# Performance work log

Hardware: AMD Instinct MI355X
Metric: run time of the kernel (lower is better)

Reference implementation:

```python
import jax, jax.numpy as jnp
import numpy as np

HEADS = 8
DIM_HEAD = 64
SCALE = DIM_HEAD ** (-0.5)
EPS = 1e-5


def setup_inputs() -> dict:
    key = jax.random.key(0)
    k1, k2, k3, k4 = jax.random.split(key, 4)
    b, c, t = 16, 512, 4096
    hidden = HEADS * DIM_HEAD
    x = jax.random.normal(k1, (b, c, t), dtype=jnp.float32)
    W_qkv = jax.random.normal(k2, (hidden * 3, c), dtype=jnp.float32) * (c ** -0.5)
    W_out = jax.random.normal(k3, (c, hidden), dtype=jnp.float32) * (hidden ** -0.5)
    b_out = jax.random.normal(k4, (c,), dtype=jnp.float32) * 0.02
    gn_w = jnp.ones((c,), dtype=jnp.float32)
    gn_b = jnp.zeros((c,), dtype=jnp.float32)
    return {"x": x, "W_qkv": W_qkv, "W_out": W_out, "b_out": b_out,
            "gn_w": gn_w, "gn_b": gn_b}


def reference(x, W_qkv, W_out, b_out, gn_w, gn_b):
    b, c, t = x.shape
    # 1x1 conv = channel matmul: [3*hidden, c] @ [b, c, t] -> [b, 3*hidden, t]
    qkv = jnp.einsum('oc,bct->bot', W_qkv, x)
    q, k, v = jnp.split(qkv, 3, axis=1)
    q = q.reshape(b, HEADS, DIM_HEAD, t)
    k = k.reshape(b, HEADS, DIM_HEAD, t)
    v = v.reshape(b, HEADS, DIM_HEAD, t)
    q = jax.nn.softmax(q, axis=-2) * SCALE  # softmax over feature dim
    k = jax.nn.softmax(k, axis=-1)          # softmax over time dim
    # context = k @ v^T : [b,h,dk,t] x [b,h,t,dv] -> [b,h,dk,dv]
    context = jnp.einsum('bhdt,bhet->bhde', k, v)
    # out = context^T @ q : [b,h,dv,dk] x [b,h,dk,t] -> [b,h,dv,t]
    out = jnp.einsum('bhde,bhdt->bhet', context, q)
    out = out.reshape(b, HEADS * DIM_HEAD, t)
    # output 1x1 conv with bias
    out = jnp.einsum('oc,bct->bot', W_out, out) + b_out[None, :, None]
    # GroupNorm(1, dim): normalize over (channels, time) per sample
    mean = jnp.mean(out, axis=(1, 2), keepdims=True)
    var = jnp.var(out, axis=(1, 2), keepdims=True)
    out = (out - mean) * jax.lax.rsqrt(var + EPS)
    out = out * gn_w[None, :, None] + gn_b[None, :, None]
    return out
```

## Files before the change

### kernel.cpp

```cpp
#include <hip/hip_runtime.h>
#include <stdint.h>

#define B_ 16
#define C_ 512
#define T_ 4096
#define H_ 8
#define D_ 64
#define SCALE_ 0.125f
#define EPS_ 1e-5f

using ushortT = unsigned short;
using ushort8 = __attribute__((ext_vector_type(8))) unsigned short;
using short8  = __attribute__((ext_vector_type(8))) short;
using floatx4 = __attribute__((ext_vector_type(4))) float;

__device__ __forceinline__ float bf2f(ushortT u) {
  union { unsigned int i; float f; } x; x.i = ((unsigned int)u) << 16; return x.f;
}
__device__ __forceinline__ ushortT f2bf(float f) {
  union { float f; unsigned int i; } x; x.f = f;
  unsigned int r = x.i + 0x7fffu + ((x.i >> 16) & 1u);
  return (ushortT)(r >> 16);
}

#define GLD16(gp, lp)                                                          \
  __builtin_amdgcn_global_load_lds(                                            \
      (const __attribute__((address_space(1))) unsigned int*)(gp),             \
      (__attribute__((address_space(3))) unsigned int*)(lp), 16, 0, 0)

__global__ __launch_bounds__(256) void cvt_f32_bf16(const float* __restrict__ src,
                                                    ushortT* __restrict__ dst, int n4) {
  int i = blockIdx.x * 256 + threadIdx.x;
  if (i >= n4) return;
  floatx4 v = *(const floatx4*)(src + (size_t)i * 4);
  unsigned int p0 = (unsigned int)f2bf(v[0]) | ((unsigned int)f2bf(v[1]) << 16);
  unsigned int p1 = (unsigned int)f2bf(v[2]) | ((unsigned int)f2bf(v[3]) << 16);
  *(unsigned long long*)(dst + (size_t)i * 4) =
      (unsigned long long)p0 | ((unsigned long long)p1 << 32);
}

__global__ void zero_f32(float* p, int n4) {
  int i = blockIdx.x * 256 + threadIdx.x;
  if (i < n4) ((floatx4*)p)[i] = (floatx4){0.f, 0.f, 0.f, 0.f};
}

__global__ __launch_bounds__(256) void transpose_x(const float* __restrict__ x,
                                                   ushortT* __restrict__ xT) {
  __shared__ ushortT tile[64][65];
  int b = blockIdx.z;
  int t0 = blockIdx.x * 64, c0 = blockIdx.y * 64;
  const float* xb = x + (size_t)b * C_ * T_;
  ushortT* xTb = xT + (size_t)b * T_ * C_;
  for (int i = threadIdx.x; i < 4096; i += 256) {
    int cc = i >> 6, tt = i & 63;
    tile[cc][tt] = f2bf(xb[(size_t)(c0 + cc) * T_ + t0 + tt]);
  }
  __syncthreads();
  for (int i = threadIdx.x; i < 4096; i += 256) {
    int tt = i >> 6, cc = i & 63;
    xTb[(size_t)(t0 + tt) * C_ + c0 + cc] = tile[cc][tt];
  }
}

#define STAGE_TILE(KB, BUF)                                                    \
  {                                                                            \
    _Pragma("unroll")                                                          \
    for (int i_ = 0; i_ < 4; ++i_) {                                           \
      int wci_ = i_ * 256 + (tid & 192);                                       \
      int ci_  = wci_ + (tid & 63);                                            \
      int row_ = ci_ >> 3;                                                     \
      int scol_ = ((ci_ & 7) ^ (row_ & 7)) << 3;                               \
      GLD16(&A[(size_t)(m0 + row_) * lda + (KB) + scol_], &As[BUF][wci_ * 8]); \
      GLD16(&Bt[(size_t)(n0 + row_) * ldb + (KB) + scol_], &Bs[BUF][wci_ * 8]);\
    }                                                                          \
  }

template <int MODE>
__global__ __launch_bounds__(256) void gemm_bt(
    const ushortT* __restrict__ A, const ushortT* __restrict__ Bt,
    void* __restrict__ Cc, const float* __restrict__ bias,
    float* __restrict__ stats,
    int K, int lda, int ldb, int ldc,
    unsigned long long bsA, unsigned long long bsB, unsigned long long bsC) {
  __shared__ ushortT As[2][128 * 64];
  __shared__ ushortT Bs[2][128 * 64];
  unsigned int gx = gridDim.x, gy = gridDim.y;
  unsigned int nwg = gx * gy * gridDim.z;
  unsigned int lin = blockIdx.x + gx * (blockIdx.y + gy * blockIdx.z);
  unsigned int cpx = nwg >> 3;
  unsigned int wid = (lin & 7u) * cpx + (lin >> 3);
  unsigned int bx = wid % gx;
  unsigned int tmp = wid / gx;
  unsigned int by = tmp % gy;
  unsigned int bz = tmp / gy;

  const int b = bz;
  A += (size_t)b * bsA; Bt += (size_t)b * bsB;
  const int m0 = by * 128, n0 = bx * 128;
  const int tid = threadIdx.x;
  const int w = tid >> 6, l = tid & 63;
  const int wm = (w >> 1) * 64, wn = (w & 1) * 64;
  const int quad = l >> 4, ln = l & 15;
  floatx4 acc[4][4];
#pragma unroll
  for (int i = 0; i < 4; i++)
#pragma unroll
    for (int j = 0; j < 4; j++) acc[i][j] = (floatx4){0.f, 0.f, 0.f, 0.f};

  STAGE_TILE(0, 0);
  const int nt = K >> 6;
  for (int t = 0; t < nt; ++t) {
    const int cur = t & 1;
    if (t + 1 < nt) {
      STAGE_TILE((t + 1) << 6, cur ^ 1);
      asm volatile("s_waitcnt vmcnt(8)" ::: "memory");
    } else {
      asm volatile("s_waitcnt vmcnt(0)" ::: "memory");
    }
    __builtin_amdgcn_s_barrier();
    asm volatile("" ::: "memory");
#pragma unroll
    for (int kk = 0; kk < 2; ++kk) {
      short8 af[4], bfv[4];
#pragma unroll
      for (int i = 0; i < 4; i++)
        af[i] = *(const short8*)(
            &As[cur][(wm + i * 16 + ln) * 64 + (((kk * 4 + quad) ^ (ln & 7)) << 3)]);
#pragma unroll
      for (int j = 0; j < 4; j++)
        bfv[j] = *(const short8*)(
            &Bs[cur][(wn + j * 16 + ln) * 64 + (((kk * 4 + quad) ^ (ln & 7)) << 3)]);
#pragma unroll
      for (int i = 0; i < 4; i++)
#pragma unroll
        for (int j = 0; j < 4; j++)
          acc[i][j] = __builtin_amdgcn_mfma_f32_16x16x32_bf16(af[i], bfv[j], acc[i][j], 0, 0, 0);
    }
    asm volatile("s_waitcnt lgkmcnt(0)" ::: "memory");
    __builtin_amdgcn_s_barrier();
    asm volatile("" ::: "memory");
  }

  if constexpr (MODE == 4) {
    const bool isk = (m0 < 512);
    ushortT* Co = (ushortT*)Cc + (size_t)b * bsC;
#pragma unroll
    for (int i = 0; i < 4; i++)
#pragma unroll
      for (int r = 0; r < 4; r++) {
        int row = m0 + wm + i * 16 + quad * 4 + r;
#pragma unroll
        for (int j = 0; j < 4; j++) {
          int col = n0 + wn + j * 16 + ln;
          float v = acc[i][j][r];
          if (isk) v = expf(v);
          Co[(size_t)row * ldc + col] = f2bf(v);
        }
      }
  } else if constexpr (MODE == 2) {
    ushortT* Co = (ushortT*)Cc + (size_t)b * bsC;
#pragma unroll
    for (int i = 0; i < 4; i++)
#pragma unroll
      for (int r = 0; r < 4; r++) {
        float v0 = acc[i][0][r], v1 = acc[i][1][r], v2 = acc[i][2][r], v3 = acc[i][3][r];
        float mx = fmaxf(fmaxf(v0, v1), fmaxf(v2, v3));
#pragma unroll
        for (int off = 1; off < 16; off <<= 1) mx = fmaxf(mx, __shfl_xor(mx, off));
        float e0 = expf(v0 - mx), e1 = expf(v1 - mx);
        float e2 = expf(v2 - mx), e3 = expf(v3 - mx);
        float s = (e0 + e1) + (e2 + e3);
#pragma unroll
        for (int off = 1; off < 16; off <<= 1) s += __shfl_xor(s, off);
        float inv = SCALE_ / s;
        int row = m0 + wm + i * 16 + quad * 4 + r;
        size_t base = (size_t)row * ldc + n0 + wn + ln;
        Co[base +  0] = f2bf(e0 * inv);
        Co[base + 16] = f2bf(e1 * inv);
        Co[base + 32] = f2bf(e2 * inv);
        Co[base + 48] = f2bf(e3 * inv);
      }
  } else {
    float* Co = (float*)Cc + (size_t)b * bsC;
    float s = 0.f, ss = 0.f;
#pragma unroll
    for (int i = 0; i < 4; i++)
#pragma unroll
      for (int r = 0; r < 4; r++) {
        int row = m0 + wm + i * 16 + quad * 4 + r;
        float bv = bias ? bias[row] : 0.f;
#pragma unroll
        for (int j = 0; j < 4; j++) {
          int col = n0 + wn + j * 16 + ln;
          float v = acc[i][j][r] + bv;
          Co[(size_t)row * ldc + col] = v;
          s += v; ss += v * v;
        }
      }
#pragma unroll
    for (int off = 1; off < 64; off <<= 1) {
      s += __shfl_xor(s, off);
      ss += __shfl_xor(ss, off);
    }
    __shared__ float rs[4], rss[4];
    if (l == 0) { rs[w] = s; rss[w] = ss; }
    __syncthreads();
    if (tid == 0) {
      atomicAdd(&stats[b * 2],     rs[0] + rs[1] + rs[2] + rs[3]);
      atomicAdd(&stats[b * 2 + 1], rss[0] + rss[1] + rss[2] + rss[3]);
    }
  }
}

__global__ __launch_bounds__(64) void context_kv(const ushortT* __restrict__ kv,
                                                 float* __restrict__ ksum,
                                                 float* __restrict__ ct) {
  __shared__ ushortT Vs[64 * 32];
  __shared__ ushortT Ks[64 * 32];
  const int slice = blockIdx.x, h = blockIdx.y, b = blockIdx.z;
  const int t0 = slice * 256;
  const ushortT* vrow = kv + ((size_t)b * 1024 + 512 + h * 64) * T_;
  const ushortT* krow = kv + ((size_t)b * 1024 + h * 64) * T_;
  const int tid = threadIdx.x, quad = tid >> 4, ln = tid & 15;
  float rsum[4] = {0.f, 0.f, 0.f, 0.f};
  floatx4 acc[4][4];
#pragma unroll
  for (int i = 0; i < 4; i++)
#pragma unroll
    for (int j = 0; j < 4; j++) acc[i][j] = (floatx4){0.f, 0.f, 0.f, 0.f};
  for (int kb = 0; kb < 256; kb += 32) {
#pragma unroll
    for (int i = 0; i < 4; ++i) {
      int ci = i * 64 + tid;
      int row = ci >> 2, col = (ci & 3) << 3;
      GLD16(&vrow[(size_t)row * T_ + t0 + kb + col], &Vs[i * 512]);
      GLD16(&krow[(size_t)row * T_ + t0 + kb + col], &Ks[i * 512]);
    }
    __syncthreads();
    short8 af[4], bfv[4];
#pragma unroll
    for (int i = 0; i < 4; i++) af[i] = *(const short8*)(&Vs[(i * 16 + ln) * 32 + quad * 8]);
#pragma unroll
    for (int j = 0; j < 4; j++) {
      bfv[j] = *(const short8*)(&Ks[(j * 16 + ln) * 32 + quad * 8]);
#pragma unroll
      for (int e = 0; e < 8; e++) rsum[j] += bf2f((ushortT)bfv[j][e]);
    }
#pragma unroll
    for (int i = 0; i < 4; i++)
#pragma unroll
      for (int j = 0; j < 4; j++)
        acc[i][j] = __builtin_amdgcn_mfma_f32_16x16x32_bf16(af[i], bfv[j], acc[i][j], 0, 0, 0);
    __syncthreads();
  }
  float* ks = ksum + (size_t)b * 512 + h * 64;
#pragma unroll
  for (int j = 0; j < 4; ++j) {
    float s = rsum[j];
    s += __shfl_xor(s, 16);
    s += __shfl_xor(s, 32);
    if (quad == 0) atomicAdd(&ks[j * 16 + ln], s);
  }
  float* ctbh = ct + (size_t)(b * 8 + h) * 4096;
#pragma unroll
  for (int i = 0; i < 4; i++)
#pragma unroll
    for (int r = 0; r < 4; r++) {
      int e = i * 16 + quad * 4 + r;
#pragma unroll
      for (int j = 0; j < 4; j++) {
        int d = j * 16 + ln;
        atomicAdd(&ctbh[e * 64 + d], acc[i][j][r]);
      }
    }
}

__global__ __launch_bounds__(64) void ct_combine(const ushortT* __restrict__ Wobf,
                                                 const float* __restrict__ ct,
                                                 const float* __restrict__ ksum,
                                                 ushortT* __restrict__ W2) {
  __shared__ ushortT As[64 * 64];
  __shared__ float Cs[64 * 64];
  const int c0 = blockIdx.x * 64, h = blockIdx.y, b = blockIdx.z;
  const int tid = threadIdx.x, quad = tid >> 4, ln = tid & 15;
  const float* ctbh = ct + (size_t)(b * 8 + h) * 4096;
#pragma unroll
  for (int i = 0; i < 8; ++i) {
    int ci = i * 64 + tid;
    int row = ci >> 3, col = (ci & 7) << 3;
    *(uint4*)(&As[row * 64 + col]) = *(const uint4*)(&Wobf[(size_t)(c0 + row) * 512 + h * 64 + col]);
  }
#pragma unroll
  for (int i = 0; i < 16; ++i) {
    int off = (i * 64 + tid) * 4;
    *(floatx4*)(&Cs[off]) = *(const floatx4*)(&ctbh[off]);
  }
  const float* ks = ksum + (size_t)b * 512 + h * 64;
  float invd[4];
#pragma unroll
  for (int j = 0; j < 4; j++) invd[j] = 1.f / ks[j * 16 + ln];
  __syncthreads();
  floatx4 acc[4][4];
#pragma unroll
  for (int i = 0; i < 4; i++)
#pragma unroll
    for (int j = 0; j < 4; j++) acc[i][j] = (floatx4){0.f, 0.f, 0.f, 0.f};
#pragma unroll
  for (int kk = 0; kk < 2; ++kk) {
    short8 af[4], bfv[4];
#pragma unroll
    for (int i = 0; i < 4; i++) af[i] = *(const short8*)(&As[(i * 16 + ln) * 64 + kk * 32 + quad * 8]);
#pragma unroll
    for (int j = 0; j < 4; j++) {
#pragma unroll
      for (int e2 = 0; e2 < 8; ++e2)
        bfv[j][e2] = (short)f2bf(Cs[(kk * 32 + quad * 8 + e2) * 64 + j * 16 + ln] * invd[j]);
    }
#pragma unroll
    for (int i = 0; i < 4; i++)
#pragma unroll
      for (int j = 0; j < 4; j++)
        acc[i][j] = __builtin_amdgcn_mfma_f32_16x16x32_bf16(af[i], bfv[j], acc[i][j], 0, 0, 0);
  }
  ushortT* W2b = W2 + (size_t)b * 512 * 512;
#pragma unroll
  for (int i = 0; i < 4; i++)
#pragma unroll
    for (int r = 0; r < 4; r++) {
      int row = c0 + i * 16 + quad * 4 + r;
#pragma unroll
      for (int j = 0; j < 4; j++) {
        int col = h * 64 + j * 16 + ln;
        W2b[(size_t)row * 512 + col] = f2bf(acc[i][j][r]);
      }
    }
}

__global__ __launch_bounds__(256) void gn_apply(float* __restrict__ out,
                                                const float* __restrict__ stats,
                                                const float* __restrict__ gnw,
                                                const float* __restrict__ gnb) {
  int b = blockIdx.y;
  int i = blockIdx.x * 256 + threadIdx.x;
  const float invN = 1.f / (float)(C_ * T_);
  float mean = stats[b * 2] * invN;
  float var = stats[b * 2 + 1] * invN - mean * mean;
  float inv = rsqrtf(var + EPS_);
  int c = i >> 9;
  float wv = gnw[c] * inv, bv = gnb[c];
  float* p = out + (size_t)b * C_ * T_ + (size_t)i * 8;
  floatx4 v0 = *(const floatx4*)p;
  floatx4 v1 = *(const floatx4*)(p + 4);
#pragma unroll
  for (int j = 0; j < 4; j++) v0[j] = (v0[j] - mean) * wv + bv;
#pragma unroll
  for (int j = 0; j < 4; j++) v1[j] = (v1[j] - mean) * wv + bv;
  *(floatx4*)p = v0;
  *(floatx4*)(p + 4) = v1;
}

extern "C" void kernel_launch(void* const* d_in, const int* in_sizes, int n_in,
                              void* d_out, int out_size, void* d_ws, size_t ws_size,
                              hipStream_t stream) {
  (void)in_sizes; (void)n_in; (void)out_size; (void)ws_size;
  const float* x    = (const float*)d_in[0];
  const float* Wqkv = (const float*)d_in[1];
  const float* Wout = (const float*)d_in[2];
  const float* bout = (const float*)d_in[3];
  const float* gnw  = (const float*)d_in[4];
  const float* gnb  = (const float*)d_in[5];
  float* out = (float*)d_out;

  char* ws = (char*)d_ws;
  ushortT* xT   = (ushortT*)(ws);
  ushortT* qT   = (ushortT*)(ws + 67108864);
  ushortT* Wqbf = (ushortT*)(ws + 134217728);
  ushortT* Wobf = (ushortT*)(ws + 135790592);
  float*   ct   = (float*)(ws + 136314880);
  float* stats  = (float*)(ws + 138412032);
  float* ksum   = (float*)(ws);
  ushortT* W2   = (ushortT*)(ws + 1048576);
  ushortT* kv   = (ushortT*)d_out;

  cvt_f32_bf16<<<768, 256, 0, stream>>>(Wqkv, Wqbf, 196608);
  cvt_f32_bf16<<<256, 256, 0, stream>>>(Wout, Wobf, 65536);
  zero_f32<<<513, 256, 0, stream>>>(ct, 131080);

  transpose_x<<<dim3(64, 8, 16), 256, 0, stream>>>(x, xT);

  gemm_bt<4><<<dim3(32, 8, 16), 256, 0, stream>>>(
      Wqbf + 512 * 512, xT, kv, nullptr, nullptr, 512, 512, 512, 4096,
      0ULL, (unsigned long long)(T_ * 512), (unsigned long long)(1024 * T_));

  gemm_bt<2><<<dim3(4, 32, 16), 256, 0, stream>>>(
      xT, Wqbf, qT, nullptr, nullptr, 512, 512, 512, 512,
      (unsigned long long)(T_ * 512), 0ULL, (unsigned long long)(T_ * 512));

  zero_f32<<<8, 256, 0, stream>>>(ksum, 2048);

  context_kv<<<dim3(16, 8, 16), 64, 0, stream>>>(kv, ksum, ct);

  ct_combine<<<dim3(8, 8, 16), 64, 0, stream>>>(Wobf, ct, ksum, W2);

  gemm_bt<3><<<dim3(32, 4, 16), 256, 0, stream>>>(
      W2, qT, out, bout, stats, 512, 512, 512, 4096,
      (unsigned long long)(512 * 512), (unsigned long long)(T_ * 512),
      (unsigned long long)(512 * T_));

  gn_apply<<<dim3(1024, 16), 256, 0, stream>>>(out, stats, gnw, gnb);
}
```

Measured before the change: 589.8 us.

## Stage only one GEMM operand in LDS, read the other directly from global

The GEMM kernel now copies only one operand tile (chosen by a template flag) into a single double-buffered shared array. The other operand's MFMA fragments are loaded straight from global memory each k-step. This halves LDS use and staging traffic, which may raise occupancy. The cost is that the direct operand is read uncoalesced and unpipelined from global/L2 inside the inner loop, and loads are repeated across waves.

```diff
diff --git a/kernel.cpp b/kernel.cpp
--- a/kernel.cpp
+++ b/kernel.cpp
@@ -62,28 +62,14 @@
   }
 }
 
-#define STAGE_TILE(KB, BUF)                                                    \
-  {                                                                            \
-    _Pragma("unroll")                                                          \
-    for (int i_ = 0; i_ < 4; ++i_) {                                           \
-      int wci_ = i_ * 256 + (tid & 192);                                       \
-      int ci_  = wci_ + (tid & 63);                                            \
-      int row_ = ci_ >> 3;                                                     \
-      int scol_ = ((ci_ & 7) ^ (row_ & 7)) << 3;                               \
-      GLD16(&A[(size_t)(m0 + row_) * lda + (KB) + scol_], &As[BUF][wci_ * 8]); \
-      GLD16(&Bt[(size_t)(n0 + row_) * ldb + (KB) + scol_], &Bs[BUF][wci_ * 8]);\
-    }                                                                          \
-  }
-
-template <int MODE>
+template <int MODE, int STAGE_A>
 __global__ __launch_bounds__(256) void gemm_bt(
     const ushortT* __restrict__ A, const ushortT* __restrict__ Bt,
     void* __restrict__ Cc, const float* __restrict__ bias,
     float* __restrict__ stats,
     int K, int lda, int ldb, int ldc,
     unsigned long long bsA, unsigned long long bsB, unsigned long long bsC) {
-  __shared__ ushortT As[2][128 * 64];
-  __shared__ ushortT Bs[2][128 * 64];
+  __shared__ ushortT Ss[2][128 * 64];
   unsigned int gx = gridDim.x, gy = gridDim.y;
   unsigned int nwg = gx * gy * gridDim.z;
   unsigned int lin = blockIdx.x + gx * (blockIdx.y + gy * blockIdx.z);
@@ -101,19 +87,42 @@
   const int w = tid >> 6, l = tid & 63;
   const int wm = (w >> 1) * 64, wn = (w & 1) * 64;
   const int quad = l >> 4, ln = l & 15;
+
+  const ushortT* Sp = STAGE_A ? A : Bt;
+  const ushortT* Dp = STAGE_A ? Bt : A;
+  const int ldS = STAGE_A ? lda : ldb;
+  const int ldD = STAGE_A ? ldb : lda;
+  const int s0  = STAGE_A ? m0 : n0;
+  const int d0  = STAGE_A ? n0 : m0;
+  const int wS  = STAGE_A ? wm : wn;
+  const int wD  = STAGE_A ? wn : wm;
+
   floatx4 acc[4][4];
 #pragma unroll
   for (int i = 0; i < 4; i++)
 #pragma unroll
     for (int j = 0; j < 4; j++) acc[i][j] = (floatx4){0.f, 0.f, 0.f, 0.f};
 
-  STAGE_TILE(0, 0);
+#define STAGE_S(KB, BUF)                                                       \
+  {                                                                            \
+    _Pragma("unroll")                                                          \
+    for (int i_ = 0; i_ < 4; ++i_) {                                           \
+      int wci_ = i_ * 256 + (tid & 192);                                       \
+      int ci_  = wci_ + (tid & 63);                                            \
+      int row_ = ci_ >> 3;                                                     \
+      int scol_ = ((ci_ & 7) ^ (row_ & 7)) << 3;                               \
+      GLD16(&Sp[(size_t)(s0 + row_) * ldS + (KB) + scol_], &Ss[BUF][wci_ * 8]);\
+    }                                                                          \
+  }
+
+  STAGE_S(0, 0);
   const int nt = K >> 6;
   for (int t = 0; t < nt; ++t) {
     const int cur = t & 1;
+    const int kb = t << 6;
     if (t + 1 < nt) {
-      STAGE_TILE((t + 1) << 6, cur ^ 1);
-      asm volatile("s_waitcnt vmcnt(8)" ::: "memory");
+      STAGE_S((t + 1) << 6, cur ^ 1);
+      asm volatile("s_waitcnt vmcnt(4)" ::: "memory");
     } else {
       asm volatile("s_waitcnt vmcnt(0)" ::: "memory");
     }
@@ -121,25 +130,27 @@
     asm volatile("" ::: "memory");
 #pragma unroll
     for (int kk = 0; kk < 2; ++kk) {
-      short8 af[4], bfv[4];
+      short8 sf[4], df[4];
 #pragma unroll
       for (int i = 0; i < 4; i++)
-        af[i] = *(const short8*)(
-            &As[cur][(wm + i * 16 + ln) * 64 + (((kk * 4 + quad) ^ (ln & 7)) << 3)]);
+        sf[i] = *(const short8*)(
+            &Ss[cur][(wS + i * 16 + ln) * 64 + (((kk * 4 + quad) ^ (ln & 7)) << 3)]);
 #pragma unroll
       for (int j = 0; j < 4; j++)
-        bfv[j] = *(const short8*)(
-            &Bs[cur][(wn + j * 16 + ln) * 64 + (((kk * 4 + quad) ^ (ln & 7)) << 3)]);
+        df[j] = *(const short8*)(
+            &Dp[(size_t)(d0 + wD + j * 16 + ln) * ldD + kb + kk * 32 + quad * 8]);
 #pragma unroll
       for (int i = 0; i < 4; i++)
 #pragma unroll
         for (int j = 0; j < 4; j++)
-          acc[i][j] = __builtin_amdgcn_mfma_f32_16x16x32_bf16(af[i], bfv[j], acc[i][j], 0, 0, 0);
+          acc[i][j] = __builtin_amdgcn_mfma_f32_16x16x32_bf16(
+              STAGE_A ? sf[i] : df[i], STAGE_A ? df[j] : sf[j], acc[i][j], 0, 0, 0);
     }
     asm volatile("s_waitcnt lgkmcnt(0)" ::: "memory");
     __builtin_amdgcn_s_barrier();
     asm volatile("" ::: "memory");
   }
+#undef STAGE_S
 
   if constexpr (MODE == 4) {
     const bool isk = (m0 < 512);
@@ -388,11 +399,11 @@
 
   transpose_x<<<dim3(64, 8, 16), 256, 0, stream>>>(x, xT);
 
-  gemm_bt<4><<<dim3(32, 8, 16), 256, 0, stream>>>(
+  gemm_bt<4, 0><<<dim3(32, 8, 16), 256, 0, stream>>>(
       Wqbf + 512 * 512, xT, kv, nullptr, nullptr, 512, 512, 512, 4096,
       0ULL, (unsigned long long)(T_ * 512), (unsigned long long)(1024 * T_));
 
-  gemm_bt<2><<<dim3(4, 32, 16), 256, 0, stream>>>(
+  gemm_bt<2, 1><<<dim3(4, 32, 16), 256, 0, stream>>>(
       xT, Wqbf, qT, nullptr, nullptr, 512, 512, 512, 512,
       (unsigned long long)(T_ * 512), 0ULL, (unsigned long long)(T_ * 512));
 
@@ -402,7 +413,7 @@
 
   ct_combine<<<dim3(8, 8, 16), 64, 0, stream>>>(Wobf, ct, ksum, W2);
 
-  gemm_bt<3><<<dim3(32, 4, 16), 256, 0, stream>>>(
+  gemm_bt<3, 0><<<dim3(32, 4, 16), 256, 0, stream>>>(
       W2, qT, out, bout, stats, 512, 512, 512, 4096,
       (unsigned long long)(512 * 512), (unsigned long long)(T_ * 512),
       (unsigned long long)(512 * T_));
```

Result: slower. 700.5 us (+18.8%).
